# Kernel optimization log

Measured on AMD Instinct MI355X. Metric: run time of the kernel, lower is better.

Reference implementation:

```python
import jax, jax.numpy as jnp
import numpy as np

N_EMBD = 512
N_HEAD = 8
HEAD_DIM = N_EMBD // N_HEAD


def setup_inputs() -> dict:
    key = jax.random.key(0)
    ks = jax.random.split(key, 10)
    B, Tx, Tc, C = 8, 1024, 2048, N_EMBD
    s = 1.0 / np.sqrt(C)
    return {
        "x": jax.random.normal(ks[0], (B, Tx, C), dtype=jnp.float32),
        "context": jax.random.normal(ks[1], (B, Tc, C), dtype=jnp.float32),
        "Wq": jax.random.normal(ks[2], (C, C), dtype=jnp.float32) * s,
        "bq": jnp.zeros((C,), dtype=jnp.float32),
        "Wk": jax.random.normal(ks[3], (C, C), dtype=jnp.float32) * s,
        "bk": jnp.zeros((C,), dtype=jnp.float32),
        "Wv": jax.random.normal(ks[4], (C, C), dtype=jnp.float32) * s,
        "bv": jnp.zeros((C,), dtype=jnp.float32),
        "Wo": jax.random.normal(ks[5], (C, C), dtype=jnp.float32) * s,
        "bo": jnp.zeros((C,), dtype=jnp.float32),
    }


def reference(x, context, Wq, bq, Wk, bk, Wv, bv, Wo, bo):
    B, Tx, C = x.shape
    Tc = context.shape[1]
    nh, hd = N_HEAD, C // N_HEAD
    # projections (torch Linear: y = x @ W.T + b)
    q = (x @ Wq.T + bq).reshape(B, Tx, nh, hd).transpose(0, 2, 1, 3)
    k = (context @ Wk.T + bk).reshape(B, Tc, nh, hd).transpose(0, 2, 1, 3)
    v = (context @ Wv.T + bv).reshape(B, Tc, nh, hd).transpose(0, 2, 1, 3)
    # attention scores (B, nh, Tx, Tc)
    att = jnp.einsum("bhqd,bhkd->bhqk", q, k) * (1.0 / np.sqrt(hd))
    att = jax.nn.softmax(att, axis=-1)
    y = jnp.einsum("bhqk,bhkd->bhqd", att, v)
    y = y.transpose(0, 2, 1, 3).reshape(B, Tx, C)
    att_mean = att.mean(axis=1)  # (B, Tx, Tc)
    y = y @ Wo.T + bo
    return (y, att_mean)
```

## Files before the change

### kernel.cpp

```cpp
#include <hip/hip_runtime.h>

#define DEVI __device__ __forceinline__

typedef short bf16x8 __attribute__((ext_vector_type(8)));
typedef short bf16x4 __attribute__((ext_vector_type(4)));
typedef float f32x4 __attribute__((ext_vector_type(4)));

constexpr int Bb = 8, TX = 1024, TC = 2048, CC = 512, NH = 8, HD = 64;
constexpr float LOG2E = 1.44269504f;

DEVI unsigned short f2bf(float f) {
  union { float f; unsigned u; } v; v.f = f;
  return (unsigned short)((v.u + 0x7FFFu + ((v.u >> 16) & 1u)) >> 16);
}

DEVI unsigned cvtpk(float lo, float hi) {
  unsigned r;
  asm("v_cvt_pk_bf16_f32 %0, %1, %2" : "=v"(r) : "v"(lo), "v"(hi));
  return r;
}

DEVI f32x4 mfma16(bf16x8 a, bf16x8 b, f32x4 c) {
  return __builtin_amdgcn_mfma_f32_16x16x32_bf16(a, b, c, 0, 0, 0);
}

DEVI f32x4 zero4() { f32x4 z = {0.f, 0.f, 0.f, 0.f}; return z; }

DEVI float max3f(float a, float b, float c) { return fmaxf(fmaxf(a, b), c); }

DEVI void gload_lds16(const unsigned short* g, unsigned short* l) {
  __builtin_amdgcn_global_load_lds(
      (const __attribute__((address_space(1))) void*)g,
      (__attribute__((address_space(3))) void*)l, 16, 0, 0);
}

DEVI void cvt_region(const float* __restrict__ src,
                     unsigned short* __restrict__ dst, int n8, int i0, int stride) {
  for (int i = i0; i < n8; i += stride) {
    f32x4 a = *(const f32x4*)(src + (size_t)i * 8);
    f32x4 b = *(const f32x4*)(src + (size_t)i * 8 + 4);
    bf16x8 v;
#pragma unroll
    for (int j = 0; j < 4; j++) {
      v[j] = (short)f2bf(a[j]);
      v[j + 4] = (short)f2bf(b[j]);
    }
    *(bf16x8*)(dst + (size_t)i * 8) = v;
  }
}

__global__ __launch_bounds__(256) void cvt_all(
    const float* __restrict__ s0, unsigned short* __restrict__ d0, int n0,
    const float* __restrict__ s1, unsigned short* __restrict__ d1, int n1,
    const float* __restrict__ s2, unsigned short* __restrict__ d2, int n2,
    const float* __restrict__ s3, unsigned short* __restrict__ d3, int n3,
    const float* __restrict__ s4, unsigned short* __restrict__ d4, int n4,
    const float* __restrict__ s5, unsigned short* __restrict__ d5, int n5) {
  const int i0 = blockIdx.x * 256 + threadIdx.x;
  const int stride = gridDim.x * 256;
  cvt_region(s0, d0, n0, i0, stride);
  cvt_region(s1, d1, n1, i0, stride);
  cvt_region(s2, d2, n2, i0, stride);
  cvt_region(s3, d3, n3, i0, stride);
  cvt_region(s4, d4, n4, i0, stride);
  cvt_region(s5, d5, n5, i0, stride);
}

template <int MODE>
__global__ __launch_bounds__(256) void gemm64m(
    const unsigned short* __restrict__ A, const unsigned short* __restrict__ W,
    const float* __restrict__ bias, void* __restrict__ outp, int tlog2, float scale) {
  __shared__ __align__(16) unsigned short As[2][64 * 32];
  __shared__ __align__(16) unsigned short Bs[2][128 * 32];

  const int tid = threadIdx.x;
  const int wid = tid >> 6, l = tid & 63, l15 = l & 15, lhi = l >> 4;
  const int wm = wid >> 1, wn = wid & 1;
  const int mbase = blockIdx.y * 64, nbase = blockIdx.x * 128;

  f32x4 acc[2][4];
#pragma unroll
  for (int i = 0; i < 2; i++)
#pragma unroll
    for (int j = 0; j < 4; j++) acc[i][j] = zero4();

  auto stage = [&](int buf, int k0) {
    {
      const int u = wid * 64 + l;
      const int row = u >> 2;
      const int gc = ((u & 3) ^ ((row >> 1) & 3)) * 8;
      gload_lds16(A + (size_t)(mbase + row) * CC + k0 + gc,
                  &As[buf][(wid * 64) * 8]);
    }
#pragma unroll
    for (int i = 0; i < 2; i++) {
      const int u = wid * 128 + i * 64 + l;
      const int row = u >> 2;
      const int gc = ((u & 3) ^ ((row >> 1) & 3)) * 8;
      gload_lds16(W + (size_t)(nbase + row) * CC + k0 + gc,
                  &Bs[buf][(wid * 128 + i * 64) * 8]);
    }
  };

  stage(0, 0);

  const int sA = (lhi ^ ((l15 >> 1) & 3)) << 3;

  constexpr int NK = CC / 32;
  for (int kt = 0; kt < NK; kt++) {
    const int cur = kt & 1;
    __syncthreads();
    if (kt + 1 < NK) stage(cur ^ 1, (kt + 1) * 32);

    bf16x8 af[2], bfr[4];
#pragma unroll
    for (int mi = 0; mi < 2; mi++)
      af[mi] = *(const bf16x8*)&As[cur][(wm * 32 + mi * 16 + l15) * 32 + sA];
#pragma unroll
    for (int ni = 0; ni < 4; ni++)
      bfr[ni] = *(const bf16x8*)&Bs[cur][(wn * 64 + ni * 16 + l15) * 32 + sA];
#pragma unroll
    for (int mi = 0; mi < 2; mi++)
#pragma unroll
      for (int ni = 0; ni < 4; ni++)
        acc[mi][ni] = mfma16(af[mi], bfr[ni], acc[mi][ni]);
  }

#pragma unroll
  for (int mi = 0; mi < 2; mi++)
#pragma unroll
    for (int ni = 0; ni < 4; ni++)
#pragma unroll
      for (int r = 0; r < 4; r++) {
        int grow = mbase + wm * 32 + mi * 16 + 4 * lhi + r;
        int gcol = nbase + wn * 64 + ni * 16 + l15;
        float val = (acc[mi][ni][r] + bias[gcol]) * scale;
        if (MODE == 0) {
          int T = 1 << tlog2;
          int bq = grow >> tlog2, tt = grow & (T - 1);
          int h = gcol >> 6, d = gcol & 63;
          size_t oidx = ((size_t)(bq * NH + h) * T + tt) * HD + d;
          ((unsigned short*)outp)[oidx] = f2bf(val);
        } else {
          ((float*)outp)[(size_t)grow * CC + gcol] = val;
        }
      }
}

__global__ __launch_bounds__(256, 2) void kv_gemm128(
    const unsigned short* __restrict__ A, const unsigned short* __restrict__ Wk,
    const unsigned short* __restrict__ Wv, const float* __restrict__ bk,
    const float* __restrict__ bv, unsigned short* __restrict__ k_out,
    unsigned short* __restrict__ v_out) {
  __shared__ __align__(16) unsigned short As[2][128 * 32];
  __shared__ __align__(16) unsigned short Bks[2][128 * 32];
  __shared__ __align__(16) unsigned short Bvs[2][128 * 32];

  const int tid = threadIdx.x;
  const int wid = tid >> 6, l = tid & 63, l15 = l & 15, lhi = l >> 4;
  const int wm = wid >> 1, wn = wid & 1;
  const int mbase = blockIdx.y * 128, nbase = blockIdx.x * 128;

  f32x4 acck[4][4], accv[4][4];
#pragma unroll
  for (int i = 0; i < 4; i++)
#pragma unroll
    for (int j = 0; j < 4; j++) { acck[i][j] = zero4(); accv[i][j] = zero4(); }

  auto stage = [&](int buf, int k0) {
#pragma unroll
    for (int i = 0; i < 2; i++) {
      const int u = wid * 128 + i * 64 + l;
      const int row = u >> 2;
      const int gc = ((u & 3) ^ ((row >> 1) & 3)) * 8;
      const int lo = (wid * 128 + i * 64) * 8;
      gload_lds16(A + (size_t)(mbase + row) * CC + k0 + gc, &As[buf][lo]);
      gload_lds16(Wk + (size_t)(nbase + row) * CC + k0 + gc, &Bks[buf][lo]);
      gload_lds16(Wv + (size_t)(nbase + row) * CC + k0 + gc, &Bvs[buf][lo]);
    }
  };

  stage(0, 0);

  const int sA = (lhi ^ ((l15 >> 1) & 3)) << 3;

  constexpr int NK = CC / 32;
  for (int kt = 0; kt < NK; kt++) {
    const int cur = kt & 1;
    __syncthreads();
    if (kt + 1 < NK) stage(cur ^ 1, (kt + 1) * 32);

    bf16x8 af[4], kf[4], vf[4];
#pragma unroll
    for (int mi = 0; mi < 4; mi++)
      af[mi] = *(const bf16x8*)&As[cur][(wm * 64 + mi * 16 + l15) * 32 + sA];
#pragma unroll
    for (int ni = 0; ni < 4; ni++) {
      kf[ni] = *(const bf16x8*)&Bks[cur][(wn * 64 + ni * 16 + l15) * 32 + sA];
      vf[ni] = *(const bf16x8*)&Bvs[cur][(wn * 64 + ni * 16 + l15) * 32 + sA];
    }
#pragma unroll
    for (int mi = 0; mi < 4; mi++)
#pragma unroll
      for (int ni = 0; ni < 4; ni++) {
        acck[mi][ni] = mfma16(af[mi], kf[ni], acck[mi][ni]);
        accv[mi][ni] = mfma16(af[mi], vf[ni], accv[mi][ni]);
      }
  }

#pragma unroll
  for (int mi = 0; mi < 4; mi++)
#pragma unroll
    for (int ni = 0; ni < 4; ni++)
#pragma unroll
      for (int r = 0; r < 4; r++) {
        int grow = mbase + wm * 64 + mi * 16 + 4 * lhi + r;
        int gcol = nbase + wn * 64 + ni * 16 + l15;
        int bq = grow >> 11, tt = grow & (TC - 1);
        int h = gcol >> 6, d = gcol & 63;
        float kv = acck[mi][ni][r] + bk[gcol];
        float vv = accv[mi][ni][r] + bv[gcol];
        k_out[((size_t)(bq * NH + h) * TC + tt) * HD + d] = f2bf(kv);
        v_out[((size_t)(bq * NH + h) * HD + d) * TC + tt] = f2bf(vv);
      }
}

__global__ __launch_bounds__(512) void attn_fwd(
    const unsigned short* __restrict__ Qw, const unsigned short* __restrict__ Kw,
    const unsigned short* __restrict__ Vtw, unsigned short* __restrict__ y_pre,
    float* __restrict__ m_ws, float* __restrict__ il_ws) {
  __shared__ __align__(16) unsigned short ktl[2][64 * 64];
  __shared__ __align__(16) unsigned short vtl[2][64 * 64];

  const int tid = threadIdx.x;
  const int wid = tid >> 6, l = tid & 63, l15 = l & 15, lhi = l >> 4;
  const int p = blockIdx.x + (TX / 128) * (blockIdx.y + NH * blockIdx.z);
  const int qg = p >> 6, h = (p >> 3) & 7, b = p & 7;
  const int qbase = qg * 128 + wid * 16;

  const unsigned short* Qh = Qw + (size_t)(b * NH + h) * TX * HD;
  const unsigned short* Kh = Kw + (size_t)(b * NH + h) * TC * HD;
  const unsigned short* Vt = Vtw + (size_t)(b * NH + h) * TC * HD;

  bf16x8 aq0 = *(const bf16x8*)(Qh + (size_t)(qbase + l15) * HD + lhi * 8);
  bf16x8 aq1 = *(const bf16x8*)(Qh + (size_t)(qbase + l15) * HD + 32 + lhi * 8);

  bf16x8 ones;
#pragma unroll
  for (int j = 0; j < 8; j++) ones[j] = (short)0x3F80;

  f32x4 accy[4];
#pragma unroll
  for (int db = 0; db < 4; db++) accy[db] = zero4();
  f32x4 accl = zero4();
  float mrun = -1e30f;

  const int sl0 = l15 + ((lhi & 1) << 5);
  const int sl1 = sl0 + 16;
  const bool sel = ((lhi >> 1) & 1) != 0;

  const int rs0 = (lhi ^ (l15 & 7)) << 3;
  const int rs1 = ((lhi ^ 4) ^ (l15 & 7)) << 3;

  const int sr = tid >> 3;
  const int ssw = ((tid & 7) ^ (sr & 7)) << 3;
  const int sc0 = (tid & 7) * 8;

  bf16x8 kr = *(const bf16x8*)(Kh + (size_t)sr * HD + sc0);
  bf16x8 vp = *(const bf16x8*)(Vt + (size_t)sr * TC + sc0);
  *(bf16x8*)&ktl[0][sr * 64 + ssw] = kr;
  *(bf16x8*)&vtl[0][sr * 64 + ssw] = vp;
  __syncthreads();

  constexpr int NT = TC / 64;
  for (int kt = 0; kt < NT; kt++) {
    const int cur = kt & 1;

    if (kt + 1 < NT) {
      const int keyn = (kt + 1) * 64;
      kr = *(const bf16x8*)(Kh + (size_t)(keyn + sr) * HD + sc0);
      vp = *(const bf16x8*)(Vt + (size_t)sr * TC + keyn + sc0);
    }

    f32x4 s[4];
    __builtin_amdgcn_s_setprio(1);
#pragma unroll
    for (int kb = 0; kb < 4; kb++) {
      bf16x8 bk0 = *(const bf16x8*)&ktl[cur][(kb * 16 + l15) * 64 + rs0];
      bf16x8 bk1 = *(const bf16x8*)&ktl[cur][(kb * 16 + l15) * 64 + rs1];
      f32x4 a = zero4();
      a = mfma16(bk0, aq0, a);
      a = mfma16(bk1, aq1, a);
      s[kb] = a;
    }
    __builtin_amdgcn_s_setprio(0);

    float t0 = max3f(s[0][0], s[0][1], s[0][2]);
    float t1 = max3f(s[0][3], s[1][0], s[1][1]);
    float t2 = max3f(s[1][2], s[1][3], s[2][0]);
    float t3 = max3f(s[2][1], s[2][2], s[2][3]);
    float t4 = max3f(s[3][0], s[3][1], s[3][2]);
    float mx = fmaxf(max3f(t0, t1, t2), max3f(t3, t4, s[3][3]));
    mx = fmaxf(mx, __shfl_xor(mx, 16));
    mx = fmaxf(mx, __shfl_xor(mx, 32));

    if (__any(mx - mrun > 7.0f)) {
      float mn = fmaxf(mrun, mx);
      float sc = exp2f(mrun - mn);
      mrun = mn;
#pragma unroll
      for (int r = 0; r < 4; r++) accl[r] *= sc;
#pragma unroll
      for (int db = 0; db < 4; db++)
#pragma unroll
        for (int r = 0; r < 4; r++) accy[db][r] *= sc;
    }

    float p4[4][4];
#pragma unroll
    for (int kb = 0; kb < 4; kb++)
#pragma unroll
      for (int r = 0; r < 4; r++) p4[kb][r] = exp2f(s[kb][r] - mrun);

    unsigned pkw[4][2];
#pragma unroll
    for (int kb = 0; kb < 4; kb++) {
      pkw[kb][0] = cvtpk(p4[kb][0], p4[kb][1]);
      pkw[kb][1] = cvtpk(p4[kb][2], p4[kb][3]);
    }
    unsigned a00 = (unsigned)__shfl((int)pkw[0][0], sl0);
    unsigned a01 = (unsigned)__shfl((int)pkw[0][1], sl0);
    unsigned a10 = (unsigned)__shfl((int)pkw[1][0], sl0);
    unsigned a11 = (unsigned)__shfl((int)pkw[1][1], sl0);
    unsigned c00 = (unsigned)__shfl((int)pkw[0][0], sl1);
    unsigned c01 = (unsigned)__shfl((int)pkw[0][1], sl1);
    unsigned c10 = (unsigned)__shfl((int)pkw[1][0], sl1);
    unsigned c11 = (unsigned)__shfl((int)pkw[1][1], sl1);
    unsigned e00 = (unsigned)__shfl((int)pkw[2][0], sl0);
    unsigned e01 = (unsigned)__shfl((int)pkw[2][1], sl0);
    unsigned e10 = (unsigned)__shfl((int)pkw[3][0], sl0);
    unsigned e11 = (unsigned)__shfl((int)pkw[3][1], sl0);
    unsigned g00 = (unsigned)__shfl((int)pkw[2][0], sl1);
    unsigned g01 = (unsigned)__shfl((int)pkw[2][1], sl1);
    unsigned g10 = (unsigned)__shfl((int)pkw[3][0], sl1);
    unsigned g11 = (unsigned)__shfl((int)pkw[3][1], sl1);
    union { unsigned u[4]; bf16x8 v; } B0, B1;
    B0.u[0] = sel ? a10 : a00;
    B0.u[1] = sel ? a11 : a01;
    B0.u[2] = sel ? c10 : c00;
    B0.u[3] = sel ? c11 : c01;
    B1.u[0] = sel ? e10 : e00;
    B1.u[1] = sel ? e11 : e01;
    B1.u[2] = sel ? g10 : g00;
    B1.u[3] = sel ? g11 : g01;

    __builtin_amdgcn_s_setprio(1);
#pragma unroll
    for (int db = 0; db < 4; db++) {
      bf16x8 bv0 = *(const bf16x8*)&vtl[cur][(db * 16 + l15) * 64 + rs0];
      bf16x8 bv1 = *(const bf16x8*)&vtl[cur][(db * 16 + l15) * 64 + rs1];
      accy[db] = mfma16(bv0, B0.v, accy[db]);
      accy[db] = mfma16(bv1, B1.v, accy[db]);
    }
    accl = mfma16(ones, B0.v, accl);
    accl = mfma16(ones, B1.v, accl);
    __builtin_amdgcn_s_setprio(0);

    if (kt + 1 < NT) {
      const int nxt = cur ^ 1;
      *(bf16x8*)&ktl[nxt][sr * 64 + ssw] = kr;
      *(bf16x8*)&vtl[nxt][sr * 64 + ssw] = vp;
    }
    __syncthreads();
  }

  const float il = 1.f / accl[0];

#pragma unroll
  for (int db = 0; db < 4; db++) {
    bf16x4 o;
#pragma unroll
    for (int r = 0; r < 4; r++) o[r] = (short)f2bf(accy[db][r] * il);
    *(bf16x4*)(y_pre + (size_t)(b * TX + qbase + l15) * CC + h * HD + db * 16 +
               4 * lhi) = o;
  }
  if (lhi == 0) {
    int idx = (b * NH + h) * TX + qbase + l15;
    m_ws[idx] = mrun;
    il_ws[idx] = il;
  }
}

__global__ __launch_bounds__(512) void att_mean_k(
    const unsigned short* __restrict__ Qw, const unsigned short* __restrict__ Kw,
    const float* __restrict__ m_ws, const float* __restrict__ il_ws,
    float* __restrict__ attm) {
  __shared__ __align__(16) unsigned short ktl[2][64 * 64];

  const int tid = threadIdx.x;
  const int wid = tid >> 6, l = tid & 63, l15 = l & 15, lhi = l >> 4;
  const int qbase = blockIdx.x * 128 + wid * 16;
  const int keyb = blockIdx.y * 64;
  const int b = blockIdx.z;

  const unsigned short* Qb = Qw + (size_t)b * NH * TX * HD;
  const unsigned short* Kb = Kw + (size_t)b * NH * TC * HD;

  const int rs0 = (lhi ^ (l15 & 7)) << 3;
  const int rs1 = ((lhi ^ 4) ^ (l15 & 7)) << 3;

  const int sr = tid >> 3;
  const int ssw = ((tid & 7) ^ (sr & 7)) << 3;
  const int sc0 = (tid & 7) * 8;

  bf16x8 aq0[2], aq1[2];
  f32x4 mm[2], ii[2];

  auto load_q = [&](int h, int p) {
    const unsigned short* qp =
        Qb + ((size_t)h * TX + qbase + l15) * HD + lhi * 8;
    aq0[p] = *(const bf16x8*)qp;
    aq1[p] = *(const bf16x8*)(qp + 32);
    mm[p] = *(const f32x4*)(m_ws + (size_t)(b * NH + h) * TX + qbase + 4 * lhi);
    ii[p] = *(const f32x4*)(il_ws + (size_t)(b * NH + h) * TX + qbase + 4 * lhi);
  };

  bf16x8 kr = *(const bf16x8*)(Kb + ((size_t)keyb + sr) * HD + sc0);
  load_q(0, 0);
  *(bf16x8*)&ktl[0][sr * 64 + ssw] = kr;
  __syncthreads();

  f32x4 am[4];
#pragma unroll
  for (int kb = 0; kb < 4; kb++) am[kb] = zero4();

#pragma unroll
  for (int h = 0; h < NH; h++) {
    const int cur = h & 1;

    if (h + 1 < NH) {
      kr = *(const bf16x8*)(Kb + ((size_t)(h + 1) * TC + keyb + sr) * HD + sc0);
      load_q(h + 1, cur ^ 1);
    }

#pragma unroll
    for (int kb = 0; kb < 4; kb++) {
      bf16x8 bk0 = *(const bf16x8*)&ktl[cur][(kb * 16 + l15) * 64 + rs0];
      bf16x8 bk1 = *(const bf16x8*)&ktl[cur][(kb * 16 + l15) * 64 + rs1];
      f32x4 a = zero4();
      a = mfma16(aq0[cur], bk0, a);
      a = mfma16(aq1[cur], bk1, a);
#pragma unroll
      for (int r = 0; r < 4; r++)
        am[kb][r] += exp2f(a[r] - mm[cur][r]) * ii[cur][r];
    }

    if (h + 1 < NH) {
      const int nxt = cur ^ 1;
      *(bf16x8*)&ktl[nxt][sr * 64 + ssw] = kr;
    }
    __syncthreads();
  }

#pragma unroll
  for (int kb = 0; kb < 4; kb++)
#pragma unroll
    for (int r = 0; r < 4; r++) {
      int trow = qbase + 4 * lhi + r;
      attm[(size_t)(b * TX + trow) * TC + keyb + kb * 16 + l15] = am[kb][r] * 0.125f;
    }
}

extern "C" void kernel_launch(void* const* d_in, const int* in_sizes, int n_in,
                              void* d_out, int out_size, void* d_ws, size_t ws_size,
                              hipStream_t stream) {
  const float* x   = (const float*)d_in[0];
  const float* ctx = (const float*)d_in[1];
  const float* Wq  = (const float*)d_in[2];
  const float* bq  = (const float*)d_in[3];
  const float* Wk  = (const float*)d_in[4];
  const float* bk  = (const float*)d_in[5];
  const float* Wv  = (const float*)d_in[6];
  const float* bv  = (const float*)d_in[7];
  const float* Wo  = (const float*)d_in[8];
  const float* bo  = (const float*)d_in[9];

  float* y_out = (float*)d_out;
  float* attm  = y_out + (size_t)Bb * TX * CC;

  unsigned short* q_ws = (unsigned short*)d_ws;
  unsigned short* k_ws = q_ws + (size_t)Bb * NH * TX * HD;
  unsigned short* v_ws = k_ws + (size_t)Bb * NH * TC * HD;
  float* m_ws  = (float*)(v_ws + (size_t)Bb * NH * TC * HD);
  float* il_ws = m_ws + (size_t)Bb * NH * TX;
  unsigned short* y_pre = (unsigned short*)(il_ws + (size_t)Bb * NH * TX);
  unsigned short* wb = y_pre + (size_t)Bb * TX * CC;
  unsigned short* wbq = wb, *wbk = wb + CC * CC, *wbv = wb + 2 * CC * CC,
                 *wbo = wb + 3 * CC * CC;

  unsigned short* xb = k_ws;
  unsigned short* cb = (unsigned short*)attm;

  const int NX8 = Bb * TX * CC / 8, NC8 = Bb * TC * CC / 8, NW8 = CC * CC / 8;
  cvt_all<<<dim3(2048), 256, 0, stream>>>(x, xb, NX8, ctx, cb, NC8,
                                          Wq, wbq, NW8, Wk, wbk, NW8,
                                          Wv, wbv, NW8, Wo, wbo, NW8);

  gemm64m<0><<<dim3(CC / 128, (Bb * TX) / 64), 256, 0, stream>>>(
      xb, wbq, bq, q_ws, 10, 0.125f * LOG2E);
  kv_gemm128<<<dim3(CC / 128, (Bb * TC) / 128), 256, 0, stream>>>(
      cb, wbk, wbv, bk, bv, k_ws, v_ws);
  attn_fwd<<<dim3(TX / 128, NH, Bb), 512, 0, stream>>>(q_ws, k_ws, v_ws, y_pre, m_ws, il_ws);
  att_mean_k<<<dim3(TX / 128, TC / 64, Bb), 512, 0, stream>>>(q_ws, k_ws, m_ws, il_ws, attm);
  gemm64m<1><<<dim3(CC / 128, (Bb * TX) / 64), 256, 0, stream>>>(
      y_pre, wbo, bo, y_out, 10, 1.0f);
}
```

Baseline: 205.0 us.

## Software-pipeline QK^T one tile ahead of softmax and PV in attention

Restructures the attention loop so the QK^T MFMAs for key tile kt are issued before the softmax and PV work for tile kt-1. This lets the exp/shuffle VALU work overlap with matrix work. The V tile buffer becomes triple-buffered because V is consumed one step later than K. The cost is extra LDS, more live registers for the two score sets, and a prologue/epilogue.

```diff
diff --git a/kernel.cpp b/kernel.cpp
--- a/kernel.cpp
+++ b/kernel.cpp
@@ -230,7 +230,7 @@
     const unsigned short* __restrict__ Vtw, unsigned short* __restrict__ y_pre,
     float* __restrict__ m_ws, float* __restrict__ il_ws) {
   __shared__ __align__(16) unsigned short ktl[2][64 * 64];
-  __shared__ __align__(16) unsigned short vtl[2][64 * 64];
+  __shared__ __align__(16) unsigned short vtl[3][64 * 64];
 
   const int tid = threadIdx.x;
   const int wid = tid >> 6, l = tid & 63, l15 = l & 15, lhi = l >> 4;
@@ -272,35 +272,15 @@
   *(bf16x8*)&vtl[0][sr * 64 + ssw] = vp;
   __syncthreads();
 
-  constexpr int NT = TC / 64;
-  for (int kt = 0; kt < NT; kt++) {
-    const int cur = kt & 1;
-
-    if (kt + 1 < NT) {
-      const int keyn = (kt + 1) * 64;
-      kr = *(const bf16x8*)(Kh + (size_t)(keyn + sr) * HD + sc0);
-      vp = *(const bf16x8*)(Vt + (size_t)sr * TC + keyn + sc0);
-    }
-
-    f32x4 s[4];
-    __builtin_amdgcn_s_setprio(1);
-#pragma unroll
-    for (int kb = 0; kb < 4; kb++) {
-      bf16x8 bk0 = *(const bf16x8*)&ktl[cur][(kb * 16 + l15) * 64 + rs0];
-      bf16x8 bk1 = *(const bf16x8*)&ktl[cur][(kb * 16 + l15) * 64 + rs1];
-      f32x4 a = zero4();
-      a = mfma16(bk0, aq0, a);
-      a = mfma16(bk1, aq1, a);
-      s[kb] = a;
-    }
-    __builtin_amdgcn_s_setprio(0);
-
-    float t0 = max3f(s[0][0], s[0][1], s[0][2]);
-    float t1 = max3f(s[0][3], s[1][0], s[1][1]);
-    float t2 = max3f(s[1][2], s[1][3], s[2][0]);
-    float t3 = max3f(s[2][1], s[2][2], s[2][3]);
-    float t4 = max3f(s[3][0], s[3][1], s[3][2]);
-    float mx = fmaxf(max3f(t0, t1, t2), max3f(t3, t4, s[3][3]));
+  f32x4 sp[4];
+
+  auto soft_pv = [&](int vbuf) {
+    float t0 = max3f(sp[0][0], sp[0][1], sp[0][2]);
+    float t1 = max3f(sp[0][3], sp[1][0], sp[1][1]);
+    float t2 = max3f(sp[1][2], sp[1][3], sp[2][0]);
+    float t3 = max3f(sp[2][1], sp[2][2], sp[2][3]);
+    float t4 = max3f(sp[3][0], sp[3][1], sp[3][2]);
+    float mx = fmaxf(max3f(t0, t1, t2), max3f(t3, t4, sp[3][3]));
     mx = fmaxf(mx, __shfl_xor(mx, 16));
     mx = fmaxf(mx, __shfl_xor(mx, 32));
 
@@ -320,7 +300,7 @@
 #pragma unroll
     for (int kb = 0; kb < 4; kb++)
 #pragma unroll
-      for (int r = 0; r < 4; r++) p4[kb][r] = exp2f(s[kb][r] - mrun);
+      for (int r = 0; r < 4; r++) p4[kb][r] = exp2f(sp[kb][r] - mrun);
 
     unsigned pkw[4][2];
 #pragma unroll
@@ -357,22 +337,72 @@
     __builtin_amdgcn_s_setprio(1);
 #pragma unroll
     for (int db = 0; db < 4; db++) {
-      bf16x8 bv0 = *(const bf16x8*)&vtl[cur][(db * 16 + l15) * 64 + rs0];
-      bf16x8 bv1 = *(const bf16x8*)&vtl[cur][(db * 16 + l15) * 64 + rs1];
+      bf16x8 bv0 = *(const bf16x8*)&vtl[vbuf][(db * 16 + l15) * 64 + rs0];
+      bf16x8 bv1 = *(const bf16x8*)&vtl[vbuf][(db * 16 + l15) * 64 + rs1];
       accy[db] = mfma16(bv0, B0.v, accy[db]);
       accy[db] = mfma16(bv1, B1.v, accy[db]);
     }
     accl = mfma16(ones, B0.v, accl);
     accl = mfma16(ones, B1.v, accl);
     __builtin_amdgcn_s_setprio(0);
+  };
+
+  constexpr int NT = TC / 64;
+
+  {
+    kr = *(const bf16x8*)(Kh + (size_t)(64 + sr) * HD + sc0);
+    vp = *(const bf16x8*)(Vt + (size_t)sr * TC + 64 + sc0);
+    __builtin_amdgcn_s_setprio(1);
+#pragma unroll
+    for (int kb = 0; kb < 4; kb++) {
+      bf16x8 bk0 = *(const bf16x8*)&ktl[0][(kb * 16 + l15) * 64 + rs0];
+      bf16x8 bk1 = *(const bf16x8*)&ktl[0][(kb * 16 + l15) * 64 + rs1];
+      f32x4 a = zero4();
+      a = mfma16(bk0, aq0, a);
+      a = mfma16(bk1, aq1, a);
+      sp[kb] = a;
+    }
+    __builtin_amdgcn_s_setprio(0);
+    *(bf16x8*)&ktl[1][sr * 64 + ssw] = kr;
+    *(bf16x8*)&vtl[1][sr * 64 + ssw] = vp;
+    __syncthreads();
+  }
+
+  for (int kt = 1; kt < NT; kt++) {
+    const int kcur = kt & 1;
 
     if (kt + 1 < NT) {
-      const int nxt = cur ^ 1;
-      *(bf16x8*)&ktl[nxt][sr * 64 + ssw] = kr;
-      *(bf16x8*)&vtl[nxt][sr * 64 + ssw] = vp;
+      const int keyn = (kt + 1) * 64;
+      kr = *(const bf16x8*)(Kh + (size_t)(keyn + sr) * HD + sc0);
+      vp = *(const bf16x8*)(Vt + (size_t)sr * TC + keyn + sc0);
+    }
+
+    f32x4 sn[4];
+    __builtin_amdgcn_s_setprio(1);
+#pragma unroll
+    for (int kb = 0; kb < 4; kb++) {
+      bf16x8 bk0 = *(const bf16x8*)&ktl[kcur][(kb * 16 + l15) * 64 + rs0];
+      bf16x8 bk1 = *(const bf16x8*)&ktl[kcur][(kb * 16 + l15) * 64 + rs1];
+      f32x4 a = zero4();
+      a = mfma16(bk0, aq0, a);
+      a = mfma16(bk1, aq1, a);
+      sn[kb] = a;
+    }
+    __builtin_amdgcn_s_setprio(0);
+
+    soft_pv((kt - 1) % 3);
+
+#pragma unroll
+    for (int kb = 0; kb < 4; kb++) sp[kb] = sn[kb];
+
+    if (kt + 1 < NT) {
+      *(bf16x8*)&ktl[(kt + 1) & 1][sr * 64 + ssw] = kr;
+      *(bf16x8*)&vtl[(kt + 1) % 3][sr * 64 + ssw] = vp;
     }
     __syncthreads();
   }
+
+  soft_pv((NT - 1) % 3);
 
   const float il = 1.f / accl[0];
 
```

After: 206.8 us. About the same (+0.9%).
